# Kernel tuning notes

Measured on AMD Instinct MI355X. Metric: run time of the kernel, lower is better.

## Reference

```python
import jax, jax.numpy as jnp
import numpy as np
from jax import lax


def setup_inputs() -> dict:
    key = jax.random.key(0)
    k1, k2 = jax.random.split(key)
    B, H, W, Cin, Cout, kh, kw = 16, 128, 128, 128, 128, 3, 3
    X = jax.random.normal(k1, (B, H, W, Cin), dtype=jnp.float32)
    kernel = jax.random.normal(k2, (B, kh, kw, Cin, Cout), dtype=jnp.float32) * 0.05
    return {"X": X, "kernel": kernel}


def _conv_one(x, k):
    # x: [H, W, Cin]; k: [kh, kw, Cin, Cout] -> [H', W', Cout]
    out = lax.conv_general_dilated(
        x[None],  # [1, H, W, Cin]
        k,
        window_strides=(1, 1),
        padding='VALID',
        dimension_numbers=('NHWC', 'HWIO', 'NHWC'),
    )
    return out[0]


def reference(X, kernel):
    # Per-sample dynamic-filter conv: each batch element convolved with its own
    # [kh, kw, Cin, Cout] filter. Equivalent to the TF depthwise-reshape trick
    # followed by reduce_sum over the input-channel axis.
    return jax.vmap(_conv_one)(X, kernel)  # [B, H', W', Cout]
```

## Files before the change

### kernel.cpp

```cpp
#include <hip/hip_runtime.h>
#include <cstdint>

#define OWD 126
#define MTOT 15876

typedef short bf16x8 __attribute__((ext_vector_type(8)));
typedef float f32x4  __attribute__((ext_vector_type(4)));

#define BT_ELEMS  (16u * 128u * 1152u)
#define XBF_ELEMS (16u * 128u * 128u * 128u)
#define WS_NEEDED ((size_t)(BT_ELEMS + XBF_ELEMS) * 2)

__device__ __forceinline__ uint16_t f2bf(float f) {
    union { float f; uint32_t u; } v;
    v.f = f;
    uint32_t u = v.u;
    return (uint16_t)((u + 0x7FFFu + ((u >> 16) & 1u)) >> 16);
}

__device__ __forceinline__ uint32_t pk2(float a, float b) {
    return (uint32_t)f2bf(a) | ((uint32_t)f2bf(b) << 16);
}

__device__ __forceinline__ void gl_lds16(const uint16_t* g, uint16_t* l) {
    __builtin_amdgcn_global_load_lds(
        (const __attribute__((address_space(1))) uint32_t*)g,
        (__attribute__((address_space(3))) uint32_t*)l, 16, 0, 0);
}

__global__ __launch_bounds__(256) void kprep(const float* __restrict__ Kin,
                                             uint16_t* __restrict__ Bt) {
    const int rs = blockIdx.x;
    const int b  = blockIdx.y;
    const int t  = threadIdx.x;
    const int n  = t & 127;
    const int og = t >> 7;

    const float* src = Kin + (((size_t)b * 9 + rs) << 14);
    uint16_t*    dst = Bt + ((size_t)b * 128 + n) * 1152 + rs * 128;

#pragma unroll
    for (int o = 0; o < 8; ++o) {
        const int oct = og * 8 + o;
        const float* s0 = src + (oct * 8) * 128 + n;
        uint4 p;
        p.x = pk2(s0[0 * 128], s0[1 * 128]);
        p.y = pk2(s0[2 * 128], s0[3 * 128]);
        p.z = pk2(s0[4 * 128], s0[5 * 128]);
        p.w = pk2(s0[6 * 128], s0[7 * 128]);
        *(uint4*)(dst + oct * 8) = p;
    }
}

__global__ __launch_bounds__(256) void xprep(const float* __restrict__ X,
                                             uint16_t* __restrict__ Xbf) {
    const size_t i = ((size_t)blockIdx.x * 256 + threadIdx.x) * 8;
    const float4 a = *(const float4*)(X + i);
    const float4 b = *(const float4*)(X + i + 4);
    uint4 p;
    p.x = pk2(a.x, a.y);
    p.y = pk2(a.z, a.w);
    p.z = pk2(b.x, b.y);
    p.w = pk2(b.z, b.w);
    *(uint4*)(Xbf + i) = p;
}

__global__ __launch_bounds__(256) void conv_mfma_c(const uint16_t* __restrict__ Xbf,
                                                   const uint16_t* __restrict__ Bt,
                                                   float* __restrict__ Out) {
    __shared__ __align__(16) uint16_t lds[3][256 * 32];

    const int id    = blockIdx.x + 125 * blockIdx.y;
    const int nid   = (id & 7) * 250 + (id >> 3);
    const int mtile = nid % 125;
    const int b     = nid / 125;

    const int tid  = threadIdx.x;
    const int lane = tid & 63;
    const int wave = tid >> 6;
    const int wm   = (wave & 1) << 6;
    const int wn   = (wave >> 1) << 6;
    const int l15  = lane & 15;
    const int quad = lane >> 4;

    const int l2 = lane >> 2;
    const int kc = (lane & 3) ^ ((lane >> 3) & 3);
    const uint16_t* Asrc[2];
    const uint16_t* Bsrc[2];
#pragma unroll
    for (int i = 0; i < 2; ++i) {
        const int row = wave * 32 + i * 16 + l2;
        int m = mtile * 128 + row;
        if (m >= MTOT) m = MTOT - 1;
        const int oh = m / OWD, ow = m - oh * OWD;
        Asrc[i] = Xbf + (((size_t)b * 128 + oh) * 128 + ow) * 128 + kc * 8;
        Bsrc[i] = Bt + ((size_t)b * 128 + row) * 1152 + kc * 8;
    }
    const int dbase = wave * 1024 + lane * 8;

    f32x4 acc[4][4];
#pragma unroll
    for (int i = 0; i < 4; ++i)
#pragma unroll
        for (int j = 0; j < 4; ++j)
            acc[i][j] = (f32x4){0.f, 0.f, 0.f, 0.f};

#define STAGE(t_, bu_)                                                      \
    {                                                                       \
        const int rs_ = (t_) >> 2;                                         \
        const int c0_ = ((t_) & 3) << 5;                                   \
        const int r_  = (rs_ * 11) >> 5;                \
        const int s_  = rs_ - r_ * 3;                                      \
        const int ao_ = (r_ * 128 + s_) * 128 + c0_;                       \
        const int bo_ = rs_ * 128 + c0_;                                   \
        uint16_t* Ad_ = &lds[bu_][dbase];                                  \
        uint16_t* Bd_ = &lds[bu_][4096 + dbase];                           \
        _Pragma("unroll")                                                  \
        for (int i_ = 0; i_ < 2; ++i_) {                                   \
            gl_lds16(Asrc[i_] + ao_, Ad_ + i_ * 512);                      \
            gl_lds16(Bsrc[i_] + bo_, Bd_ + i_ * 512);                      \
        }                                                                  \
    }

#define COMPUTE(bu_)                                                        \
    {                                                                       \
        bf16x8 af[4], bfr[4];                                              \
        _Pragma("unroll")                                                  \
        for (int i_ = 0; i_ < 4; ++i_) {                                   \
            const int row_ = wm + i_ * 16 + l15;                           \
            const int sl_  = quad ^ ((row_ >> 1) & 3);                     \
            af[i_] = *(const bf16x8*)&lds[bu_][row_ * 32 + sl_ * 8];       \
        }                                                                  \
        _Pragma("unroll")                                                  \
        for (int j_ = 0; j_ < 4; ++j_) {                                   \
            const int row_ = wn + j_ * 16 + l15;                           \
            const int sl_  = quad ^ ((row_ >> 1) & 3);                     \
            bfr[j_] = *(const bf16x8*)&lds[bu_][4096 + row_ * 32 + sl_ * 8];\
        }                                                                  \
        _Pragma("unroll")                                                  \
        for (int i_ = 0; i_ < 4; ++i_)                                     \
            _Pragma("unroll")                                              \
            for (int j_ = 0; j_ < 4; ++j_)                                 \
                acc[i_][j_] = __builtin_amdgcn_mfma_f32_16x16x32_bf16(     \
                    af[i_], bfr[j_], acc[i_][j_], 0, 0, 0);                \
    }

#define WAITBAR4                                                            \
    asm volatile("s_waitcnt vmcnt(4)" ::: "memory");                       \
    __builtin_amdgcn_s_barrier();                                          \
    __builtin_amdgcn_sched_barrier(0);

#define ITER(t_, bc_, bs_)                                                  \
    {                                                                       \
        WAITBAR4;                                                          \
        STAGE((t_) + 2, bs_);                                              \
        COMPUTE(bc_);                                                      \
    }

    STAGE(0, 0);
    STAGE(1, 1);

#pragma unroll 1
    for (int t = 0; t < 33; t += 3) {
        ITER(t, 0, 2);
        ITER(t + 1, 1, 0);
        ITER(t + 2, 2, 1);
    }
    ITER(33, 0, 2);
    WAITBAR4;
    COMPUTE(1);
    asm volatile("s_waitcnt vmcnt(0)" ::: "memory");
    __builtin_amdgcn_s_barrier();
    __builtin_amdgcn_sched_barrier(0);
    COMPUTE(2);

#undef STAGE
#undef COMPUTE
#undef WAITBAR4
#undef ITER

#pragma unroll
    for (int i = 0; i < 4; ++i) {
#pragma unroll
        for (int rr = 0; rr < 4; ++rr) {
            const int mrow = mtile * 128 + wm + i * 16 + quad * 4 + rr;
            if (mrow < MTOT) {
                const int oh2 = mrow / OWD;
                const int ow2 = mrow - oh2 * OWD;
                float* op = Out + (((size_t)b * OWD + oh2) * OWD + ow2) * 128 + wn + l15;
#pragma unroll
                for (int j = 0; j < 4; ++j)
                    op[j * 16] = acc[i][j][rr];
            }
        }
    }
}

__global__ __launch_bounds__(256) void conv_mfma(const float* __restrict__ X,
                                                 const uint16_t* __restrict__ Bt,
                                                 float* __restrict__ Out) {
    __shared__ __align__(16) uint16_t lA[128 * 64];
    __shared__ __align__(16) uint16_t lB[128 * 64];

    const int mtile = blockIdx.x;
    const int b     = blockIdx.y;
    const int tid   = threadIdx.x;
    const int lane  = tid & 63;
    const int wave  = tid >> 6;
    const int wm    = (wave & 1) << 6;
    const int wn    = (wave >> 1) << 6;
    const int l15   = lane & 15;
    const int quad  = lane >> 4;

    const int srow  = tid >> 1;
    const int shalf = tid & 1;

    int m = mtile * 128 + srow;
    if (m >= MTOT) m = MTOT - 1;
    const int oh = m / OWD;
    const int ow = m - oh * OWD;
    const float*    Xb = X + (((size_t)b * 128 + oh) * 128 + ow) * 128;
    const uint16_t* Bb = Bt + ((size_t)b * 128 + srow) * 1152 + shalf * 32;

    f32x4 acc[4][4];
#pragma unroll
    for (int i = 0; i < 4; ++i)
#pragma unroll
        for (int j = 0; j < 4; ++j)
            acc[i][j] = (f32x4){0.f, 0.f, 0.f, 0.f};

    for (int chunk = 0; chunk < 18; ++chunk) {
        const int rs = chunk >> 1;
        const int c0 = (chunk & 1) << 6;
        const int r  = rs / 3;
        const int s  = rs - r * 3;

        __syncthreads();
        {
            const float4* src = (const float4*)(Xb + (r * 128 + s) * 128 + c0 + shalf * 32);
            float4 v[8];
#pragma unroll
            for (int i = 0; i < 8; ++i) v[i] = src[i];
#pragma unroll
            for (int i = 0; i < 4; ++i) {
                uint4 p;
                p.x = pk2(v[2 * i].x, v[2 * i].y);
                p.y = pk2(v[2 * i].z, v[2 * i].w);
                p.z = pk2(v[2 * i + 1].x, v[2 * i + 1].y);
                p.w = pk2(v[2 * i + 1].z, v[2 * i + 1].w);
                const int ci = (shalf * 4 + i) ^ (srow & 7);
                *(uint4*)&lA[srow * 64 + ci * 8] = p;
            }
        }
        {
            const uint4* bsrc = (const uint4*)(Bb + rs * 128 + c0);
#pragma unroll
            for (int i = 0; i < 4; ++i) {
                const uint4 p = bsrc[i];
                const int ci = (shalf * 4 + i) ^ (srow & 7);
                *(uint4*)&lB[srow * 64 + ci * 8] = p;
            }
        }
        __syncthreads();

#pragma unroll
        for (int ksub = 0; ksub < 2; ++ksub) {
            bf16x8 af[4], bfr[4];
#pragma unroll
            for (int i = 0; i < 4; ++i) {
                const int row = wm + i * 16 + l15;
                const int ci  = (ksub * 4 + quad) ^ (row & 7);
                af[i] = *(const bf16x8*)&lA[row * 64 + ci * 8];
            }
#pragma unroll
            for (int j = 0; j < 4; ++j) {
                const int row = wn + j * 16 + l15;
                const int ci  = (ksub * 4 + quad) ^ (row & 7);
                bfr[j] = *(const bf16x8*)&lB[row * 64 + ci * 8];
            }
#pragma unroll
            for (int i = 0; i < 4; ++i)
#pragma unroll
                for (int j = 0; j < 4; ++j)
                    acc[i][j] = __builtin_amdgcn_mfma_f32_16x16x32_bf16(
                        af[i], bfr[j], acc[i][j], 0, 0, 0);
        }
    }

#pragma unroll
    for (int i = 0; i < 4; ++i) {
#pragma unroll
        for (int rr = 0; rr < 4; ++rr) {
            const int mrow = mtile * 128 + wm + i * 16 + quad * 4 + rr;
            if (mrow < MTOT) {
                const int oh2 = mrow / OWD;
                const int ow2 = mrow - oh2 * OWD;
                float* op = Out + (((size_t)b * OWD + oh2) * OWD + ow2) * 128 + wn + l15;
#pragma unroll
                for (int j = 0; j < 4; ++j)
                    op[j * 16] = acc[i][j][rr];
            }
        }
    }
}

extern "C" void kernel_launch(void* const* d_in, const int* in_sizes, int n_in,
                              void* d_out, int out_size, void* d_ws, size_t ws_size,
                              hipStream_t stream) {
    const float* X   = (const float*)d_in[0];
    const float* Kin = (const float*)d_in[1];
    float*       Out = (float*)d_out;
    uint16_t*    Bt  = (uint16_t*)d_ws;
    uint16_t*    Xbf = Bt + BT_ELEMS;

    kprep<<<dim3(9, 16), 256, 0, stream>>>(Kin, Bt);
    if (ws_size >= WS_NEEDED) {
        xprep<<<XBF_ELEMS / (256 * 8), 256, 0, stream>>>(X, Xbf);
        conv_mfma_c<<<dim3(125, 16), 256, 0, stream>>>(Xbf, Bt, Out);
    } else {
        conv_mfma<<<dim3(125, 16), 256, 0, stream>>>(X, Bt, Out);
    }
}
```

Measured before the change: 322.7 us.

## Load B fragments directly from pre-swizzled global layout into registers, bypassing LDS

Kernel prep now writes the per-sample filter in an MFMA-fragment-ordered layout, so each lane can load its B operand straight from global memory into registers. The B tile is no longer staged through LDS. This halves LDS usage per block and allows launch_bounds occupancy of 3. It also adds a triple-buffered register pipeline for B alongside the existing LDS pipeline for A. The cost is extra vector registers and per-wave global loads of B that are duplicated across the two M-waves and rely on cache hits.

Result: slower. 331.2 us (+2.6%).

```diff
diff --git a/kernel.cpp b/kernel.cpp
--- a/kernel.cpp
+++ b/kernel.cpp
@@ -30,6 +30,35 @@
 
 __global__ __launch_bounds__(256) void kprep(const float* __restrict__ Kin,
                                              uint16_t* __restrict__ Bt) {
+    const int rs = blockIdx.x;
+    const int b  = blockIdx.y;
+    const int t  = threadIdx.x;
+    const int n  = t & 127;
+    const int og = t >> 7;
+
+    const float* src = Kin + (((size_t)b * 9 + rs) << 14);
+    const int jt  = n >> 4;
+    const int l15 = n & 15;
+
+#pragma unroll
+    for (int o = 0; o < 8; ++o) {
+        const int oct = og * 8 + o;
+        const float* s0 = src + (oct * 8) * 128 + n;
+        uint4 p;
+        p.x = pk2(s0[0 * 128], s0[1 * 128]);
+        p.y = pk2(s0[2 * 128], s0[3 * 128]);
+        p.z = pk2(s0[4 * 128], s0[5 * 128]);
+        p.w = pk2(s0[6 * 128], s0[7 * 128]);
+        const int chunk = rs * 4 + (oct >> 2);
+        const int quad  = oct & 3;
+        uint16_t* d = Bt +
+            (((((size_t)b * 8 + jt) * 36 + chunk) * 16 + l15) * 4 + quad) * 8;
+        *(uint4*)d = p;
+    }
+}
+
+__global__ __launch_bounds__(256) void kprep_old(const float* __restrict__ Kin,
+                                                 uint16_t* __restrict__ Bt) {
     const int rs = blockIdx.x;
     const int b  = blockIdx.y;
     const int t  = threadIdx.x;
@@ -65,10 +94,10 @@
     *(uint4*)(Xbf + i) = p;
 }
 
-__global__ __launch_bounds__(256) void conv_mfma_c(const uint16_t* __restrict__ Xbf,
-                                                   const uint16_t* __restrict__ Bt,
-                                                   float* __restrict__ Out) {
-    __shared__ __align__(16) uint16_t lds[3][256 * 32];
+__global__ __launch_bounds__(256, 3) void conv_mfma_d(const uint16_t* __restrict__ Xbf,
+                                                      const uint16_t* __restrict__ Bt,
+                                                      float* __restrict__ Out) {
+    __shared__ __align__(16) uint16_t lds[3][128 * 32];
 
     const int id    = blockIdx.x + 125 * blockIdx.y;
     const int nid   = (id & 7) * 250 + (id >> 3);
@@ -86,7 +115,6 @@
     const int l2 = lane >> 2;
     const int kc = (lane & 3) ^ ((lane >> 3) & 3);
     const uint16_t* Asrc[2];
-    const uint16_t* Bsrc[2];
 #pragma unroll
     for (int i = 0; i < 2; ++i) {
         const int row = wave * 32 + i * 16 + l2;
@@ -94,9 +122,14 @@
         if (m >= MTOT) m = MTOT - 1;
         const int oh = m / OWD, ow = m - oh * OWD;
         Asrc[i] = Xbf + (((size_t)b * 128 + oh) * 128 + ow) * 128 + kc * 8;
-        Bsrc[i] = Bt + ((size_t)b * 128 + row) * 1152 + kc * 8;
     }
     const int dbase = wave * 1024 + lane * 8;
+
+    const uint16_t* Bp[4];
+#pragma unroll
+    for (int j = 0; j < 4; ++j)
+        Bp[j] = Bt + ((((size_t)b * 8 + (wn >> 4) + j) * 36 * 16 * 4)
+                      + ((size_t)l15 * 4 + quad)) * 8;
 
     f32x4 acc[4][4];
 #pragma unroll
@@ -104,6 +137,8 @@
 #pragma unroll
         for (int j = 0; j < 4; ++j)
             acc[i][j] = (f32x4){0.f, 0.f, 0.f, 0.f};
+
+    bf16x8 rB0[4], rB1[4], rB2[4];
 
 #define STAGE(t_, bu_)                                                      \
     {                                                                       \
@@ -112,19 +147,22 @@
         const int r_  = (rs_ * 11) >> 5;                \
         const int s_  = rs_ - r_ * 3;                                      \
         const int ao_ = (r_ * 128 + s_) * 128 + c0_;                       \
-        const int bo_ = rs_ * 128 + c0_;                                   \
         uint16_t* Ad_ = &lds[bu_][dbase];                                  \
-        uint16_t* Bd_ = &lds[bu_][4096 + dbase];                           \
         _Pragma("unroll")                                                  \
-        for (int i_ = 0; i_ < 2; ++i_) {                                   \
+        for (int i_ = 0; i_ < 2; ++i_)                                     \
             gl_lds16(Asrc[i_] + ao_, Ad_ + i_ * 512);                      \
-            gl_lds16(Bsrc[i_] + bo_, Bd_ + i_ * 512);                      \
-        }                                                                  \
-    }
-
-#define COMPUTE(bu_)                                                        \
+    }
+
+#define LOADB(t_, r_)                                                       \
     {                                                                       \
-        bf16x8 af[4], bfr[4];                                              \
+        _Pragma("unroll")                                                  \
+        for (int j_ = 0; j_ < 4; ++j_)                                     \
+            r_[j_] = *(const bf16x8*)(Bp[j_] + (size_t)(t_) * 512);        \
+    }
+
+#define COMPUTE(bu_, r_)                                                    \
+    {                                                                       \
+        bf16x8 af[4];                                                      \
         _Pragma("unroll")                                                  \
         for (int i_ = 0; i_ < 4; ++i_) {                                   \
             const int row_ = wm + i_ * 16 + l15;                           \
@@ -132,51 +170,47 @@
             af[i_] = *(const bf16x8*)&lds[bu_][row_ * 32 + sl_ * 8];       \
         }                                                                  \
         _Pragma("unroll")                                                  \
-        for (int j_ = 0; j_ < 4; ++j_) {                                   \
-            const int row_ = wn + j_ * 16 + l15;                           \
-            const int sl_  = quad ^ ((row_ >> 1) & 3);                     \
-            bfr[j_] = *(const bf16x8*)&lds[bu_][4096 + row_ * 32 + sl_ * 8];\
-        }                                                                  \
-        _Pragma("unroll")                                                  \
         for (int i_ = 0; i_ < 4; ++i_)                                     \
             _Pragma("unroll")                                              \
             for (int j_ = 0; j_ < 4; ++j_)                                 \
                 acc[i_][j_] = __builtin_amdgcn_mfma_f32_16x16x32_bf16(     \
-                    af[i_], bfr[j_], acc[i_][j_], 0, 0, 0);                \
-    }
-
-#define WAITBAR4                                                            \
-    asm volatile("s_waitcnt vmcnt(4)" ::: "memory");                       \
+                    af[i_], r_[j_], acc[i_][j_], 0, 0, 0);                 \
+    }
+
+#define WAITBAR(n_)                                                         \
+    asm volatile("s_waitcnt vmcnt(" #n_ ")" ::: "memory");                 \
     __builtin_amdgcn_s_barrier();                                          \
     __builtin_amdgcn_sched_barrier(0);
 
-#define ITER(t_, bc_, bs_)                                                  \
+#define ITER(t_, rc_, rl_, bc_, bl_)                                        \
     {                                                                       \
-        WAITBAR4;                                                          \
-        STAGE((t_) + 2, bs_);                                              \
-        COMPUTE(bc_);                                                      \
-    }
-
+        WAITBAR(6);                                                        \
+        LOADB((t_) + 2, rl_);                                              \
+        STAGE((t_) + 2, bl_);                                              \
+        COMPUTE(bc_, rc_);                                                 \
+    }
+
+    LOADB(0, rB0);
     STAGE(0, 0);
+    LOADB(1, rB1);
     STAGE(1, 1);
 
 #pragma unroll 1
     for (int t = 0; t < 33; t += 3) {
-        ITER(t, 0, 2);
-        ITER(t + 1, 1, 0);
-        ITER(t + 2, 2, 1);
-    }
-    ITER(33, 0, 2);
-    WAITBAR4;
-    COMPUTE(1);
-    asm volatile("s_waitcnt vmcnt(0)" ::: "memory");
-    __builtin_amdgcn_s_barrier();
-    __builtin_amdgcn_sched_barrier(0);
-    COMPUTE(2);
+        ITER(t,     rB0, rB2, 0, 2);
+        ITER(t + 1, rB1, rB0, 1, 0);
+        ITER(t + 2, rB2, rB1, 2, 1);
+    }
+    ITER(33, rB0, rB2, 0, 2);
+    WAITBAR(6);
+    COMPUTE(1, rB1);
+    WAITBAR(0);
+    COMPUTE(2, rB2);
 
 #undef STAGE
+#undef LOADB
 #undef COMPUTE
-#undef WAITBAR4
+#undef WAITBAR
 #undef ITER
 
 #pragma unroll
@@ -313,11 +347,12 @@
     uint16_t*    Bt  = (uint16_t*)d_ws;
     uint16_t*    Xbf = Bt + BT_ELEMS;
 
-    kprep<<<dim3(9, 16), 256, 0, stream>>>(Kin, Bt);
     if (ws_size >= WS_NEEDED) {
+        kprep<<<dim3(9, 16), 256, 0, stream>>>(Kin, Bt);
         xprep<<<XBF_ELEMS / (256 * 8), 256, 0, stream>>>(X, Xbf);
-        conv_mfma_c<<<dim3(125, 16), 256, 0, stream>>>(Xbf, Bt, Out);
+        conv_mfma_d<<<dim3(125, 16), 256, 0, stream>>>(Xbf, Bt, Out);
     } else {
+        kprep_old<<<dim3(9, 16), 256, 0, stream>>>(Kin, Bt);
         conv_mfma<<<dim3(125, 16), 256, 0, stream>>>(X, Bt, Out);
     }
 }
```
